# Performance work log

Hardware: AMD Instinct MI355X
Metric: run time of the kernel (lower is better)

Reference implementation:

```python
import jax, jax.numpy as jnp
import numpy as np

B, S, D, H, E = 4, 2048, 2048, 4096, 8
TOP_K = 2
ENTROPY_WEIGHT = 0.1
MAX_USAGE_RATIO = 0.3


def setup_inputs() -> dict:
    key = jax.random.key(0)
    k0, k1, k2 = jax.random.split(key, 3)
    x = jax.random.normal(k0, (B, S, D), dtype=jnp.float32)
    gate_w = jax.random.normal(k1, (E, D), dtype=jnp.float32) * 0.02
    gate_b = jnp.zeros((E,), dtype=jnp.float32)
    expert_w = jax.random.normal(k2, (E, H, D), dtype=jnp.float32) * 0.02
    expert_b = jnp.zeros((E, H), dtype=jnp.float32)
    return {"x": x, "gate_w": gate_w, "gate_b": gate_b,
            "expert_w": expert_w, "expert_b": expert_b}


def reference(x, gate_w, gate_b, expert_w, expert_b):
    b, s, d = x.shape
    e, h, _ = expert_w.shape
    n = b * s
    xf = x.reshape(n, d)

    # gating
    gate_logits = xf @ gate_w.T + gate_b              # (N, E)
    gate_probs = jax.nn.softmax(gate_logits, axis=-1)
    entropy = (-jnp.sum(gate_probs * jnp.log(gate_probs + 1e-10), axis=-1)).mean()
    entropy_loss = ENTROPY_WEIGHT * entropy

    # top-k dispatch weights
    topk_probs, topk_idx = jax.lax.top_k(gate_probs, TOP_K)   # (N, K)
    combine = jnp.sum(jax.nn.one_hot(topk_idx, e, dtype=xf.dtype)
                      * topk_probs[..., None], axis=1)        # (N, E)

    # per-expert linear + weighted combine (loop over small fixed E)
    out = jnp.zeros((n, h), dtype=xf.dtype)
    for ei in range(e):
        out = out + combine[:, ei:ei + 1] * (xf @ expert_w[ei].T + expert_b[ei])

    # usage penalty (this batch's routing counts)
    counts = jnp.sum(jax.nn.one_hot(topk_idx, e, dtype=jnp.float32), axis=(0, 1))
    usage_ratios = counts / n
    overuse_penalty = jnp.sum(jax.nn.relu(usage_ratios - MAX_USAGE_RATIO))

    return out.reshape(b, s, h), entropy_loss + overuse_penalty
```

## Files before the change

### kernel.cpp

```cpp
#include <hip/hip_runtime.h>

constexpr int N_TOK = 8192;
constexpr int D_IN  = 2048;
constexpr int H_OUT = 4096;
constexpr int NEXP  = 8;
constexpr float ENT_W = 0.1f;
constexpr float MAX_USAGE = 0.3f;

constexpr int TM = 128;
constexpr int TH = 128;
constexpr int BK = 64;
constexpr int NKT = D_IN / BK;
constexpr int TILES_H = H_OUT / TH;
constexpr int TM_MAX  = N_TOK / TM;
constexpr int REGION  = 8192;
constexpr int BUFSZ   = TM * BK;

typedef __attribute__((ext_vector_type(8))) short bf16x8;
typedef __attribute__((ext_vector_type(4))) float f32x4;

__device__ __forceinline__ short f2bf(float f) {
    unsigned u = __float_as_uint(f);
    u += 0x7FFF + ((u >> 16) & 1);
    return (short)(u >> 16);
}

__device__ __forceinline__ void gload16(const void* g, void* l) {
    __builtin_amdgcn_global_load_lds(
        (const __attribute__((address_space(1))) unsigned int*)g,
        (__attribute__((address_space(3))) unsigned int*)l, 16, 0, 0);
}

__global__ __launch_bounds__(256) void cvt_kernel(
    const float* __restrict__ in, short* __restrict__ out, int n8)
{
    int stride = gridDim.x * 256;
    for (int i = blockIdx.x * 256 + threadIdx.x; i < n8; i += stride) {
        const float4* p = (const float4*)in + (size_t)i * 2;
        float4 a = p[0], b = p[1];
        bf16x8 v;
        v[0] = f2bf(a.x); v[1] = f2bf(a.y); v[2] = f2bf(a.z); v[3] = f2bf(a.w);
        v[4] = f2bf(b.x); v[5] = f2bf(b.y); v[6] = f2bf(b.z); v[7] = f2bf(b.w);
        *(bf16x8*)(out + (size_t)i * 8) = v;
    }
}

__global__ __launch_bounds__(256) void gate_kernel(
    const float* __restrict__ x, const float* __restrict__ gate_w,
    const float* __restrict__ gate_b, int* __restrict__ topk_idx,
    float* __restrict__ topk_w, float* __restrict__ ent_partial,
    short* __restrict__ xb)
{
    __shared__ float ent_s[4];
    const int wv = threadIdx.x >> 6;
    const int lane = threadIdx.x & 63;
    const int t = blockIdx.x * 4 + wv;

    float acc[NEXP];
#pragma unroll
    for (int e = 0; e < NEXP; ++e) acc[e] = 0.f;

    const float4* xr = (const float4*)(x + (size_t)t * D_IN);
    short* xbr = xb + (size_t)t * D_IN;
#pragma unroll
    for (int i = 0; i < D_IN / 256; ++i) {
        float4 xv = xr[lane + i * 64];
        short4 s4;
        s4.x = f2bf(xv.x); s4.y = f2bf(xv.y); s4.z = f2bf(xv.z); s4.w = f2bf(xv.w);
        *(short4*)(xbr + i * 256 + lane * 4) = s4;
#pragma unroll
        for (int e = 0; e < NEXP; ++e) {
            float4 gv = ((const float4*)(gate_w + e * D_IN))[lane + i * 64];
            acc[e] += xv.x * gv.x + xv.y * gv.y + xv.z * gv.z + xv.w * gv.w;
        }
    }
#pragma unroll
    for (int e = 0; e < NEXP; ++e)
#pragma unroll
        for (int m = 32; m >= 1; m >>= 1) acc[e] += __shfl_xor(acc[e], m, 64);

    if (lane == 0) {
        float lg[NEXP], p[NEXP];
        float mx = -1e30f;
#pragma unroll
        for (int e = 0; e < NEXP; ++e) { lg[e] = acc[e] + gate_b[e]; mx = fmaxf(mx, lg[e]); }
        float s = 0.f;
#pragma unroll
        for (int e = 0; e < NEXP; ++e) { p[e] = expf(lg[e] - mx); s += p[e]; }
        float inv = 1.f / s;
        float ent = 0.f;
#pragma unroll
        for (int e = 0; e < NEXP; ++e) { p[e] *= inv; ent -= p[e] * logf(p[e] + 1e-10f); }
        int e1 = 0; float b1 = p[0];
#pragma unroll
        for (int e = 1; e < NEXP; ++e) if (p[e] > b1) { b1 = p[e]; e1 = e; }
        int e2 = (e1 == 0) ? 1 : 0; float b2 = p[e2];
#pragma unroll
        for (int e = 0; e < NEXP; ++e)
            if (e != e1 && e != ((e1 == 0) ? 1 : 0) && p[e] > b2) { b2 = p[e]; e2 = e; }
        topk_idx[2 * t]     = e1;  topk_idx[2 * t + 1] = e2;
        topk_w[2 * t]       = b1;  topk_w[2 * t + 1]   = b2;
        ent_s[wv] = ent;
    }
    __syncthreads();
    if (threadIdx.x == 0)
        ent_partial[blockIdx.x] = ent_s[0] + ent_s[1] + ent_s[2] + ent_s[3];
}

__global__ __launch_bounds__(256) void scatter_kernel(
    const int* __restrict__ topk_idx, const float* __restrict__ topk_w,
    int* __restrict__ cursors, int* __restrict__ tok_list,
    float* __restrict__ w_list)
{
    __shared__ int lcnt[NEXP], lbase[NEXP];
    const int tid = threadIdx.x;
    const int t = blockIdx.x * 256 + tid;
    if (tid < NEXP) lcnt[tid] = 0;
    __syncthreads();
    int e0 = topk_idx[2 * t], e1 = topk_idx[2 * t + 1];
    float w0 = topk_w[2 * t], w1 = topk_w[2 * t + 1];
    int p0 = atomicAdd(&lcnt[e0], 1);
    int p1 = atomicAdd(&lcnt[e1], 1);
    __syncthreads();
    if (tid < NEXP) lbase[tid] = atomicAdd(&cursors[tid], lcnt[tid]);
    __syncthreads();
    int d0 = e0 * REGION + lbase[e0] + p0;
    int d1 = e1 * REGION + lbase[e1] + p1;
    tok_list[d0] = t;  w_list[d0] = w0;
    tok_list[d1] = t;  w_list[d1] = w1;
}

__global__ __launch_bounds__(256) void finalize_kernel(
    const int* __restrict__ counts, const float* __restrict__ ent_partial,
    float* __restrict__ loss_out)
{
    __shared__ float red[256];
    float s = 0.f;
    for (int i = threadIdx.x; i < N_TOK / 4; i += 256) s += ent_partial[i];
    red[threadIdx.x] = s;
    __syncthreads();
    for (int st = 128; st > 0; st >>= 1) {
        if (threadIdx.x < st) red[threadIdx.x] += red[threadIdx.x + st];
        __syncthreads();
    }
    if (threadIdx.x == 0) {
        float loss = ENT_W * red[0] / (float)N_TOK;
        for (int e = 0; e < NEXP; ++e) {
            float r = (float)counts[e] / (float)N_TOK - MAX_USAGE;
            if (r > 0.f) loss += r;
        }
        loss_out[0] = loss;
    }
}

__global__ __launch_bounds__(256) void moe_gemm(
    const short* __restrict__ xb, const short* __restrict__ wb,
    const float* __restrict__ expert_b, const int* __restrict__ tok_list,
    const float* __restrict__ w_list, const int* __restrict__ counts,
    float* __restrict__ out)
{
    const int bid = blockIdx.x;
    const int e   = bid / (TM_MAX * TILES_H);
    const int rem = bid % (TM_MAX * TILES_H);
    const int tm  = rem / TILES_H;
    const int th  = rem % TILES_H;

    const int cnt = counts[e];
    if (tm * TM >= cnt) return;
    const int valid = cnt - tm * TM;
    const int hbase = th * TH;

    __shared__ __align__(16) short A_s[2][BUFSZ];
    __shared__ __align__(16) short B_s[2][BUFSZ];
    __shared__ int   tok_s[TM];
    __shared__ float wgt_s[TM];

    const int tid = threadIdx.x;
    if (tid < TM) {
        bool v = tid < valid;
        int src = e * REGION + tm * TM + tid;
        tok_s[tid] = v ? tok_list[src] : 0;
        wgt_s[tid] = v ? w_list[src] : 0.f;
    }
    __syncthreads();

    const int lane = tid & 63;
    const int wv = tid >> 6;

    const char* asrc[4];
    const char* bsrc[4];
    int dst_off[4];
#pragma unroll
    for (int j = 0; j < 4; ++j) {
        int c = wv * 4 + j;
        int r = c * 8 + (lane >> 3);
        int c16 = (lane & 7) ^ (r & 7);
        asrc[j] = (const char*)(xb + (size_t)tok_s[r] * D_IN) + c16 * 16;
        bsrc[j] = (const char*)(wb + ((size_t)e * H_OUT + hbase + r) * D_IN) + c16 * 16;
        dst_off[j] = c * 512;
    }

    const int rr = lane & 15, kg = lane >> 4;
    const int wr = wv >> 1, wc = wv & 1;

    int aoff[4][2], boff[4][2];
#pragma unroll
    for (int mi = 0; mi < 4; ++mi)
#pragma unroll
        for (int k2 = 0; k2 < 2; ++k2) {
            int row = wr * 64 + mi * 16 + rr;
            int c16 = (k2 * 4 + kg) ^ (row & 7);
            aoff[mi][k2] = row * 64 + c16 * 8;
            int rowb = wc * 64 + mi * 16 + rr;
            int c16b = (k2 * 4 + kg) ^ (rowb & 7);
            boff[mi][k2] = rowb * 64 + c16b * 8;
        }

    f32x4 acc[4][4] = {};

#pragma unroll
    for (int j = 0; j < 4; ++j) {
        gload16(asrc[j], (short*)A_s[0] + dst_off[j]); asrc[j] += BK * 2;
        gload16(bsrc[j], (short*)B_s[0] + dst_off[j]); bsrc[j] += BK * 2;
    }
#pragma unroll
    for (int j = 0; j < 4; ++j) {
        gload16(asrc[j], (short*)A_s[1] + dst_off[j]); asrc[j] += BK * 2;
        gload16(bsrc[j], (short*)B_s[1] + dst_off[j]); bsrc[j] += BK * 2;
    }
    asm volatile("s_waitcnt vmcnt(8)" ::: "memory");
    __builtin_amdgcn_sched_barrier(0);
    __builtin_amdgcn_s_barrier();

    for (int kt = 0; kt < NKT; ++kt) {
        const short* Ac = A_s[kt & 1];
        const short* Bc = B_s[kt & 1];
        short* An = (short*)A_s[kt & 1];
        short* Bn = (short*)B_s[kt & 1];

        bf16x8 af[4][2], bv[4][2];
#pragma unroll
        for (int k2 = 0; k2 < 2; ++k2) {
#pragma unroll
            for (int mi = 0; mi < 4; ++mi) af[mi][k2] = *(const bf16x8*)&Ac[aoff[mi][k2]];
#pragma unroll
            for (int ni = 0; ni < 4; ++ni) bv[ni][k2] = *(const bf16x8*)&Bc[boff[ni][k2]];
        }
        asm volatile("s_waitcnt lgkmcnt(0)" ::: "memory");
        __builtin_amdgcn_sched_barrier(0);
        __builtin_amdgcn_s_barrier();

        if (kt + 2 < NKT) {
#pragma unroll
            for (int j = 0; j < 4; ++j) {
                gload16(asrc[j], An + dst_off[j]); asrc[j] += BK * 2;
                gload16(bsrc[j], Bn + dst_off[j]); bsrc[j] += BK * 2;
            }
        }

        __builtin_amdgcn_s_setprio(1);
#pragma unroll
        for (int k2 = 0; k2 < 2; ++k2)
#pragma unroll
            for (int mi = 0; mi < 4; ++mi)
#pragma unroll
                for (int ni = 0; ni < 4; ++ni)
                    acc[mi][ni] = __builtin_amdgcn_mfma_f32_16x16x32_bf16(
                        af[mi][k2], bv[ni][k2], acc[mi][ni], 0, 0, 0);
        __builtin_amdgcn_s_setprio(0);

        if (kt + 2 < NKT) {
            asm volatile("s_waitcnt vmcnt(8)" ::: "memory");
        } else if (kt + 1 < NKT) {
            asm volatile("s_waitcnt vmcnt(0)" ::: "memory");
        }
        __builtin_amdgcn_sched_barrier(0);
        __builtin_amdgcn_s_barrier();
    }

    const float* bias = expert_b + (size_t)e * H_OUT + hbase;
#pragma unroll
    for (int mi = 0; mi < 4; ++mi) {
#pragma unroll
        for (int ni = 0; ni < 4; ++ni) {
            int col = wc * 64 + ni * 16 + rr;
            float be = bias[col];
#pragma unroll
            for (int i = 0; i < 4; ++i) {
                int r = wr * 64 + mi * 16 + kg * 4 + i;
                if (r < valid) {
                    float val = wgt_s[r] * (acc[mi][ni][i] + be);
                    atomicAdd(&out[(size_t)tok_s[r] * H_OUT + hbase + col], val);
                }
            }
        }
    }
}

extern "C" void kernel_launch(void* const* d_in, const int* in_sizes, int n_in,
                              void* d_out, int out_size, void* d_ws, size_t ws_size,
                              hipStream_t stream) {
    const float* x        = (const float*)d_in[0];
    const float* gate_w   = (const float*)d_in[1];
    const float* gate_b   = (const float*)d_in[2];
    const float* expert_w = (const float*)d_in[3];
    const float* expert_b = (const float*)d_in[4];
    float* out = (float*)d_out;
    char* ws = (char*)d_ws;

    int*   topk_idx    = (int*)(ws);
    float* topk_w      = (float*)(ws + (64 << 10));
    int*   cursors     = (int*)(ws + (128 << 10));
    float* ent_partial = (float*)(ws + (128 << 10) + 256);
    int*   tok_list    = (int*)(ws + (160 << 10));
    float* w_list      = (float*)(ws + (416 << 10));
    short* xb          = (short*)(ws + (1ull << 20));
    short* wb          = (short*)(ws + (34ull << 20));

    hipMemsetAsync(cursors, 0, 64, stream);
    hipMemsetAsync(d_out, 0, (size_t)out_size * sizeof(float), stream);

    gate_kernel<<<N_TOK / 4, 256, 0, stream>>>(x, gate_w, gate_b, topk_idx,
                                               topk_w, ent_partial, xb);
    cvt_kernel<<<4096, 256, 0, stream>>>(expert_w, wb, (NEXP * H_OUT * D_IN) / 8);
    scatter_kernel<<<N_TOK / 256, 256, 0, stream>>>(topk_idx, topk_w, cursors,
                                                    tok_list, w_list);
    finalize_kernel<<<1, 256, 0, stream>>>(cursors, ent_partial,
                                           out + (size_t)N_TOK * H_OUT);
    moe_gemm<<<NEXP * TM_MAX * TILES_H, 256, 0, stream>>>(
        xb, wb, expert_b, tok_list, w_list, cursors, out);
}
```

Measured before the change: 719.7 us.

## Pre-swizzle expert weights into MFMA fragment layout and load B directly to registers

The bf16 conversion of expert weights now writes them in a layout that matches the per-lane MFMA B-fragment order. The GEMM then loads B fragments straight from global memory into registers, bypassing LDS and halving shared memory use. The GEMM also reorders block indexing so consecutive blocks share an H tile, and raises launch bounds to request 3 blocks per CU. In exchange, B loads are no longer double-buffered through LDS, so global latency sits directly in front of the MFMAs within the same iteration, and the conversion kernel does strided reads.

```diff
diff --git a/kernel.cpp b/kernel.cpp
--- a/kernel.cpp
+++ b/kernel.cpp
@@ -31,17 +31,30 @@
         (__attribute__((address_space(3))) unsigned int*)l, 16, 0, 0);
 }
 
-__global__ __launch_bounds__(256) void cvt_kernel(
-    const float* __restrict__ in, short* __restrict__ out, int n8)
-{
-    int stride = gridDim.x * 256;
-    for (int i = blockIdx.x * 256 + threadIdx.x; i < n8; i += stride) {
-        const float4* p = (const float4*)in + (size_t)i * 2;
-        float4 a = p[0], b = p[1];
+#define LOADB(dst, base, OFF) \
+    asm volatile("global_load_dwordx4 %0, %1, off offset:" #OFF \
+                 : "=v"(dst) : "v"(base) : "memory")
+
+__global__ __launch_bounds__(256) void cvt_wb(
+    const float* __restrict__ in, short* __restrict__ out)
+{
+    const size_t total = (size_t)NEXP * 32 * 256 * 2 * 64;
+    size_t stride = (size_t)gridDim.x * 256;
+    for (size_t d = (size_t)blockIdx.x * 256 + threadIdx.x; d < total; d += stride) {
+        int lane = d & 63;
+        int k2   = (d >> 6) & 1;
+        int hgrp = (d >> 7) & 255;
+        int kt   = (d >> 15) & 31;
+        int e    = (int)(d >> 20);
+        int kg = lane >> 4, rr = lane & 15;
+        int h = hgrp * 16 + rr;
+        int k = kt * 64 + k2 * 32 + kg * 8;
+        const float4* s = (const float4*)(in + ((size_t)e * H_OUT + h) * D_IN + k);
+        float4 a = s[0], b = s[1];
         bf16x8 v;
         v[0] = f2bf(a.x); v[1] = f2bf(a.y); v[2] = f2bf(a.z); v[3] = f2bf(a.w);
         v[4] = f2bf(b.x); v[5] = f2bf(b.y); v[6] = f2bf(b.z); v[7] = f2bf(b.w);
-        *(bf16x8*)(out + (size_t)i * 8) = v;
+        *(bf16x8*)(out + d * 8) = v;
     }
 }
 
@@ -153,8 +166,8 @@
     }
 }
 
-__global__ __launch_bounds__(256) void moe_gemm(
-    const short* __restrict__ xb, const short* __restrict__ wb,
+__global__ __launch_bounds__(256, 3) void moe_gemm(
+    const short* __restrict__ xb, const short* __restrict__ wb2,
     const float* __restrict__ expert_b, const int* __restrict__ tok_list,
     const float* __restrict__ w_list, const int* __restrict__ counts,
     float* __restrict__ out)
@@ -162,8 +175,8 @@
     const int bid = blockIdx.x;
     const int e   = bid / (TM_MAX * TILES_H);
     const int rem = bid % (TM_MAX * TILES_H);
-    const int tm  = rem / TILES_H;
-    const int th  = rem % TILES_H;
+    const int th  = rem / TM_MAX;
+    const int tm  = rem % TM_MAX;
 
     const int cnt = counts[e];
     if (tm * TM >= cnt) return;
@@ -171,7 +184,6 @@
     const int hbase = th * TH;
 
     __shared__ __align__(16) short A_s[2][BUFSZ];
-    __shared__ __align__(16) short B_s[2][BUFSZ];
     __shared__ int   tok_s[TM];
     __shared__ float wgt_s[TM];
 
@@ -188,7 +200,6 @@
     const int wv = tid >> 6;
 
     const char* asrc[4];
-    const char* bsrc[4];
     int dst_off[4];
 #pragma unroll
     for (int j = 0; j < 4; ++j) {
@@ -196,14 +207,13 @@
         int r = c * 8 + (lane >> 3);
         int c16 = (lane & 7) ^ (r & 7);
         asrc[j] = (const char*)(xb + (size_t)tok_s[r] * D_IN) + c16 * 16;
-        bsrc[j] = (const char*)(wb + ((size_t)e * H_OUT + hbase + r) * D_IN) + c16 * 16;
         dst_off[j] = c * 512;
     }
 
     const int rr = lane & 15, kg = lane >> 4;
     const int wr = wv >> 1, wc = wv & 1;
 
-    int aoff[4][2], boff[4][2];
+    int aoff[4][2];
 #pragma unroll
     for (int mi = 0; mi < 4; ++mi)
 #pragma unroll
@@ -211,41 +221,49 @@
             int row = wr * 64 + mi * 16 + rr;
             int c16 = (k2 * 4 + kg) ^ (row & 7);
             aoff[mi][k2] = row * 64 + c16 * 8;
-            int rowb = wc * 64 + mi * 16 + rr;
-            int c16b = (k2 * 4 + kg) ^ (rowb & 7);
-            boff[mi][k2] = rowb * 64 + c16b * 8;
-        }
+        }
+
+    unsigned long long b0 =
+        (unsigned long long)(uintptr_t)wb2 +
+        (((unsigned long long)e * 8192 + (unsigned long long)(th * 8 + wc * 4)) * 128
+         + lane) * 16ull;
+    unsigned long long b1 = b0 + 4096;
 
     f32x4 acc[4][4] = {};
 
 #pragma unroll
     for (int j = 0; j < 4; ++j) {
         gload16(asrc[j], (short*)A_s[0] + dst_off[j]); asrc[j] += BK * 2;
-        gload16(bsrc[j], (short*)B_s[0] + dst_off[j]); bsrc[j] += BK * 2;
     }
 #pragma unroll
     for (int j = 0; j < 4; ++j) {
         gload16(asrc[j], (short*)A_s[1] + dst_off[j]); asrc[j] += BK * 2;
-        gload16(bsrc[j], (short*)B_s[1] + dst_off[j]); bsrc[j] += BK * 2;
-    }
-    asm volatile("s_waitcnt vmcnt(8)" ::: "memory");
+    }
+    asm volatile("s_waitcnt vmcnt(4)" ::: "memory");
     __builtin_amdgcn_sched_barrier(0);
     __builtin_amdgcn_s_barrier();
 
     for (int kt = 0; kt < NKT; ++kt) {
         const short* Ac = A_s[kt & 1];
-        const short* Bc = B_s[kt & 1];
         short* An = (short*)A_s[kt & 1];
-        short* Bn = (short*)B_s[kt & 1];
-
-        bf16x8 af[4][2], bv[4][2];
-#pragma unroll
-        for (int k2 = 0; k2 < 2; ++k2) {
-#pragma unroll
-            for (int mi = 0; mi < 4; ++mi) af[mi][k2] = *(const bf16x8*)&Ac[aoff[mi][k2]];
-#pragma unroll
-            for (int ni = 0; ni < 4; ++ni) bv[ni][k2] = *(const bf16x8*)&Bc[boff[ni][k2]];
-        }
+
+        bf16x8 bv[4][2];
+        LOADB(bv[0][0], b0, 0);
+        LOADB(bv[0][1], b0, 1024);
+        LOADB(bv[1][0], b0, 2048);
+        LOADB(bv[1][1], b0, 3072);
+        LOADB(bv[2][0], b1, 0);
+        LOADB(bv[2][1], b1, 1024);
+        LOADB(bv[3][0], b1, 2048);
+        LOADB(bv[3][1], b1, 3072);
+        b0 += 524288ull;  b1 += 524288ull;
+
+        bf16x8 af[4][2];
+#pragma unroll
+        for (int k2 = 0; k2 < 2; ++k2)
+#pragma unroll
+            for (int mi = 0; mi < 4; ++mi)
+                af[mi][k2] = *(const bf16x8*)&Ac[aoff[mi][k2]];
         asm volatile("s_waitcnt lgkmcnt(0)" ::: "memory");
         __builtin_amdgcn_sched_barrier(0);
         __builtin_amdgcn_s_barrier();
@@ -254,9 +272,12 @@
 #pragma unroll
             for (int j = 0; j < 4; ++j) {
                 gload16(asrc[j], An + dst_off[j]); asrc[j] += BK * 2;
-                gload16(bsrc[j], Bn + dst_off[j]); bsrc[j] += BK * 2;
             }
-        }
+            asm volatile("s_waitcnt vmcnt(4)" ::: "memory");
+        } else {
+            asm volatile("s_waitcnt vmcnt(0)" ::: "memory");
+        }
+        __builtin_amdgcn_sched_barrier(0);
 
         __builtin_amdgcn_s_setprio(1);
 #pragma unroll
@@ -269,12 +290,6 @@
                         af[mi][k2], bv[ni][k2], acc[mi][ni], 0, 0, 0);
         __builtin_amdgcn_s_setprio(0);
 
-        if (kt + 2 < NKT) {
-            asm volatile("s_waitcnt vmcnt(8)" ::: "memory");
-        } else if (kt + 1 < NKT) {
-            asm volatile("s_waitcnt vmcnt(0)" ::: "memory");
-        }
-        __builtin_amdgcn_sched_barrier(0);
         __builtin_amdgcn_s_barrier();
     }
 
@@ -315,18 +330,18 @@
     int*   tok_list    = (int*)(ws + (160 << 10));
     float* w_list      = (float*)(ws + (416 << 10));
     short* xb          = (short*)(ws + (1ull << 20));
-    short* wb          = (short*)(ws + (34ull << 20));
+    short* wb2         = (short*)(ws + (34ull << 20));
 
     hipMemsetAsync(cursors, 0, 64, stream);
     hipMemsetAsync(d_out, 0, (size_t)out_size * sizeof(float), stream);
 
     gate_kernel<<<N_TOK / 4, 256, 0, stream>>>(x, gate_w, gate_b, topk_idx,
                                                topk_w, ent_partial, xb);
-    cvt_kernel<<<4096, 256, 0, stream>>>(expert_w, wb, (NEXP * H_OUT * D_IN) / 8);
+    cvt_wb<<<8192, 256, 0, stream>>>(expert_w, wb2);
     scatter_kernel<<<N_TOK / 256, 256, 0, stream>>>(topk_idx, topk_w, cursors,
                                                     tok_list, w_list);
     finalize_kernel<<<1, 256, 0, stream>>>(cursors, ent_partial,
                                            out + (size_t)N_TOK * H_OUT);
     moe_gemm<<<NEXP * TM_MAX * TILES_H, 256, 0, stream>>>(
-        xb, wb, expert_b, tok_list, w_list, cursors, out);
-}
+        xb, wb2, expert_b, tok_list, w_list, cursors, out);
+}
```

Measured after the change: 1.041 ms. 44.7% more time.
